# Kernel tuning notes

Hardware: AMD Instinct MI355X
Metric: run time of the kernel (lower is better)

## Reference

```python
import jax, jax.numpy as jnp
import numpy as np

NEG_SLOPE = 0.2

def _smlp(x, w, b):
    # torch nn.Linear convention: y = x @ w.T + b, then leaky_relu(0.2)
    return jax.nn.leaky_relu(x @ w.T + b, NEG_SLOPE)

_gather = jax.vmap(lambda a, i: a[i])  # (N,C),(N,k) -> (N,k,C), vmapped over batch

def _lfa(points, feats, idx, w, b):
    # points: (B,N,3), feats: (B,N,F_D), idx: (B,N,k)
    knn_p = _gather(points, idx)                      # (B,N,k,3)
    rel = points[:, :, None, :] - knn_p               # (B,N,k,3)
    dist = jnp.linalg.norm(rel, axis=-1, keepdims=True)
    geo = jnp.concatenate([rel, dist], axis=-1)       # (B,N,k,4)
    mlp = _smlp(geo, w, b)                            # (B,N,k,d)
    knn_f = _gather(feats, idx)                       # (B,N,k,F_D)
    return jnp.concatenate([mlp, knn_f], axis=-1).mean(axis=2)  # (B,N,d+F_D)

def setup_inputs() -> dict:
    key = jax.random.key(0)
    ks = jax.random.split(key, 12)
    B, N, K, D = 2, 65536, 32, 64
    pts = jax.random.normal(ks[0], (B, N, 3), jnp.float32)
    feats = jax.random.normal(ks[1], (B, N, D), jnp.float32)
    idx = jax.random.randint(ks[2], (B, N, K), 0, N)
    def lin(k, o, i):
        bound = 1.0 / np.sqrt(i)
        kw, kb = jax.random.split(k)
        return (jax.random.uniform(kw, (o, i), jnp.float32, -bound, bound),
                jax.random.uniform(kb, (o,), jnp.float32, -bound, bound))
    w_init, b_init = lin(ks[3], D // 4, D)
    w_lfa1, b_lfa1 = lin(ks[4], D // 4, 4)
    w_lfa2, b_lfa2 = lin(ks[5], D // 2, 4)
    w_final, b_final = lin(ks[6], D, D)
    w_res, b_res = lin(ks[7], D, D)
    return {"points": pts, "features": feats, "knn_indices": idx,
            "w_init": w_init, "b_init": b_init,
            "w_lfa1": w_lfa1, "b_lfa1": b_lfa1,
            "w_lfa2": w_lfa2, "b_lfa2": b_lfa2,
            "w_final": w_final, "b_final": b_final,
            "w_res": w_res, "b_res": b_res}

def reference(points, features, knn_indices, w_init, b_init,
              w_lfa1, b_lfa1, w_lfa2, b_lfa2,
              w_final, b_final, w_res, b_res):
    x = _smlp(features, w_init, b_init)               # (B,N,16)
    x = _lfa(points, x, knn_indices, w_lfa1, b_lfa1)  # (B,N,32)
    x = _lfa(points, x, knn_indices, w_lfa2, b_lfa2)  # (B,N,64)
    x = _smlp(x, w_final, b_final)                    # (B,N,64)
    residual = _smlp(features, w_res, b_res)          # (B,N,64)
    return x + residual
```

## Files before the change

kernel.cpp:

```cpp
#include <hip/hip_runtime.h>
#include <math.h>

#define NPTS 65536

typedef unsigned short ushort_t;
typedef unsigned int uint_t;
typedef __attribute__((ext_vector_type(8))) short bf16x8;
typedef __attribute__((ext_vector_type(4))) float f32x4;
typedef __attribute__((ext_vector_type(2))) float f32x2;

__device__ __forceinline__ float lrelu(float x) {
  return fmaxf(x, 0.2f * x);
}
__device__ __forceinline__ f32x2 lrelu2(f32x2 s) {
  return __builtin_elementwise_max(s, s * 0.2f);
}
__device__ __forceinline__ float fast_sqrtf(float x) {
  return __builtin_amdgcn_sqrtf(x);
}
__device__ __forceinline__ ushort_t f2b(float f) {
  union { float f; uint_t u; } v; v.f = f;
  uint_t u = v.u + (0x7fffu + ((v.u >> 16) & 1u));
  return (ushort_t)(u >> 16);
}
__device__ __forceinline__ float b2f_lo(uint_t u) {
  union { uint_t u; float f; } v; v.u = u << 16; return v.f;
}
__device__ __forceinline__ float b2f_hi(uint_t u) {
  union { uint_t u; float f; } v; v.u = u & 0xffff0000u; return v.f;
}
__device__ __forceinline__ bf16x8 cvt8(const float* p) {
  float4 a = ((const float4*)p)[0];
  float4 b = ((const float4*)p)[1];
  float f[8] = {a.x, a.y, a.z, a.w, b.x, b.y, b.z, b.w};
  bf16x8 r;
#pragma unroll
  for (int j = 0; j < 8; ++j) r[j] = (short)f2b(f[j]);
  return r;
}

__device__ __forceinline__ int swz_pbase(int ppb) {
  int bid = blockIdx.x;
  if ((int)gridDim.x * ppb == 2 * NPTS) {
    int g = bid >> 3, x = bid & 7;
    return (x >> 2) * NPTS + (g * 4 + (x & 3)) * ppb;
  }
  return bid * ppb;
}

__global__ __launch_bounds__(256) void k_init(
    const float* __restrict__ feats, const float* __restrict__ w,
    const float* __restrict__ bia, ushort_t* __restrict__ x1,
    const float* __restrict__ pts, float4* __restrict__ pts4,
    const float* __restrict__ wf, const float* __restrict__ wr,
    ushort_t* __restrict__ wfb, ushort_t* __restrict__ wrb, int BN) {
  __shared__ float wt[64 * 16];
  int t = threadIdx.x;
  if (blockIdx.x < 2) {
    const float* src = blockIdx.x ? wr : wf;
    ushort_t* dst = blockIdx.x ? wrb : wfb;
    for (int e = t; e < 4096; e += 256) dst[e] = f2b(src[e]);
  }
  for (int e = t; e < 1024; e += 256) {
    int o = e >> 6, i = e & 63;
    wt[i * 16 + o] = w[e];
  }
  __syncthreads();
  int p = blockIdx.x * 256 + t;
  if (p >= BN) return;
  const float* pp = pts + (size_t)p * 3;
  pts4[p] = make_float4(pp[0], pp[1], pp[2], 0.0f);
  float acc[16];
#pragma unroll
  for (int o = 0; o < 16; ++o) acc[o] = bia[o];
  const float4* xr4 = (const float4*)(feats + (size_t)p * 64);
#pragma unroll 4
  for (int i4 = 0; i4 < 16; ++i4) {
    float4 xv = xr4[i4];
    float xs[4] = {xv.x, xv.y, xv.z, xv.w};
#pragma unroll
    for (int s = 0; s < 4; ++s) {
      float xi = xs[s];
      const float4* w4 = (const float4*)&wt[(i4 * 4 + s) * 16];
#pragma unroll
      for (int q = 0; q < 4; ++q) {
        float4 wv = w4[q];
        acc[q * 4 + 0] = fmaf(xi, wv.x, acc[q * 4 + 0]);
        acc[q * 4 + 1] = fmaf(xi, wv.y, acc[q * 4 + 1]);
        acc[q * 4 + 2] = fmaf(xi, wv.z, acc[q * 4 + 2]);
        acc[q * 4 + 3] = fmaf(xi, wv.w, acc[q * 4 + 3]);
      }
    }
  }
  union { ushort_t u[16]; uint4 v[2]; } pk;
#pragma unroll
  for (int o = 0; o < 16; ++o) pk.u[o] = f2b(lrelu(acc[o]));
  uint4* op = (uint4*)(x1 + (size_t)p * 16);
  op[0] = pk.v[0];
  op[1] = pk.v[1];
}

__global__ __launch_bounds__(256) void k_lfa1g(
    const float4* __restrict__ pts4, const ushort_t* __restrict__ fin,
    const int* __restrict__ idx, const float* __restrict__ w1,
    const float* __restrict__ b1, const float* __restrict__ w2,
    const float* __restrict__ b2, ushort_t* __restrict__ x2out,
    ushort_t* __restrict__ g2out, int BN) {
  int t = threadIdx.x;
  int p = swz_pbase(32) + (t >> 3);
  int sub = t & 7;
  if (p >= BN) return;
  int base = p & ~(NPTS - 1);
  float4 mp = pts4[p];
  const float* w1b = w1 + sub * 8;
  f32x2 w1p[4], b1p;
#pragma unroll
  for (int k = 0; k < 4; ++k) w1p[k] = f32x2{w1b[k], w1b[4 + k]};
  b1p = f32x2{b1[sub * 2], b1[sub * 2 + 1]};
  const float* w2b = w2 + sub * 16;
  f32x2 w2p[2][4], b2p[2];
#pragma unroll
  for (int pr = 0; pr < 2; ++pr) {
#pragma unroll
    for (int k = 0; k < 4; ++k)
      w2p[pr][k] = f32x2{w2b[pr * 8 + k], w2b[pr * 8 + 4 + k]};
    b2p[pr] = f32x2{b2[sub * 4 + pr * 2], b2[sub * 4 + pr * 2 + 1]};
  }
  f32x2 m1 = {0.f, 0.f}, f1 = {0.f, 0.f};
  f32x2 m2[2] = {{0.f, 0.f}, {0.f, 0.f}};
  const int4* iv4 = (const int4*)(idx + (size_t)p * 32);
#pragma unroll 2
  for (int kk = 0; kk < 8; ++kk) {
    int4 iv = iv4[kk];
    int js[4] = {iv.x, iv.y, iv.z, iv.w};
#pragma unroll
    for (int u = 0; u < 4; ++u) {
      int j = base + js[u];
      float4 pj = pts4[j];
      uint_t fv = *((const uint_t*)(fin + (size_t)j * 16) + sub);
      float rx = mp.x - pj.x, ry = mp.y - pj.y, rz = mp.z - pj.z;
      float d = fast_sqrtf(fmaf(rx, rx, fmaf(ry, ry, rz * rz)));
      f32x2 vx = {rx, rx}, vy = {ry, ry}, vz = {rz, rz}, vd = {d, d};
      f32x2 s = __builtin_elementwise_fma(vd, w1p[3], b1p);
      s = __builtin_elementwise_fma(vz, w1p[2], s);
      s = __builtin_elementwise_fma(vy, w1p[1], s);
      s = __builtin_elementwise_fma(vx, w1p[0], s);
      m1 += lrelu2(s);
#pragma unroll
      for (int pr = 0; pr < 2; ++pr) {
        f32x2 s2 = __builtin_elementwise_fma(vd, w2p[pr][3], b2p[pr]);
        s2 = __builtin_elementwise_fma(vz, w2p[pr][2], s2);
        s2 = __builtin_elementwise_fma(vy, w2p[pr][1], s2);
        s2 = __builtin_elementwise_fma(vx, w2p[pr][0], s2);
        m2[pr] += lrelu2(s2);
      }
      f1 += f32x2{b2f_lo(fv), b2f_hi(fv)};
    }
  }
  const float inv = 1.0f / 32.0f;
  ushort_t* orow = x2out + (size_t)p * 32;
  union { ushort_t u[2]; uint_t v; } pm, pf;
  pm.u[0] = f2b(m1.x * inv); pm.u[1] = f2b(m1.y * inv);
  pf.u[0] = f2b(f1.x * inv); pf.u[1] = f2b(f1.y * inv);
  ((uint_t*)orow)[sub] = pm.v;
  ((uint_t*)orow)[8 + sub] = pf.v;
  union { ushort_t u[4]; uint2 v; } pg;
  pg.u[0] = f2b(m2[0].x * inv); pg.u[1] = f2b(m2[0].y * inv);
  pg.u[2] = f2b(m2[1].x * inv); pg.u[3] = f2b(m2[1].y * inv);
  ((uint2*)(g2out + (size_t)p * 32))[sub] = pg.v;
}

__global__ __launch_bounds__(256) void k_lfa2f(
    const ushort_t* __restrict__ fin, const int* __restrict__ idx,
    const ushort_t* __restrict__ g2, const float* __restrict__ feats,
    const ushort_t* __restrict__ wfb, const float* __restrict__ bfi,
    const ushort_t* __restrict__ wrb, const float* __restrict__ bri,
    float* __restrict__ out, int BN) {
  int t = threadIdx.x;
  int lane = t & 63, wave = t >> 6;
  int n = lane & 15, quad = lane >> 4;
  int wbase = swz_pbase(64) + wave * 16;
  int p0 = wbase + n;
  int p = p0 < BN ? p0 : BN - 1;
  int base = p & ~(NPTS - 1);
  f32x2 fa[4];
#pragma unroll
  for (int o = 0; o < 4; ++o) fa[o] = f32x2{0.f, 0.f};
  const int4* iv4 = (const int4*)(idx + (size_t)p * 32);
#pragma unroll 8
  for (int kk = 0; kk < 8; ++kk) {
    int4 iv = iv4[kk];
    int js[4] = {iv.x, iv.y, iv.z, iv.w};
#pragma unroll
    for (int u = 0; u < 4; ++u) {
      int j = base + js[u];
      uint4 fv = *((const uint4*)(fin + (size_t)j * 32) + quad);
      fa[0] += f32x2{b2f_lo(fv.x), b2f_hi(fv.x)};
      fa[1] += f32x2{b2f_lo(fv.y), b2f_hi(fv.y)};
      fa[2] += f32x2{b2f_lo(fv.z), b2f_hi(fv.z)};
      fa[3] += f32x2{b2f_lo(fv.w), b2f_hi(fv.w)};
    }
  }
  const float inv = 1.0f / 32.0f;
  bf16x8 Ax0 = *((const bf16x8*)(g2 + (size_t)p * 32 + quad * 8));
  bf16x8 Ax1;
#pragma unroll
  for (int o = 0; o < 4; ++o) {
    Ax1[o * 2 + 0] = (short)f2b(fa[o].x * inv);
    Ax1[o * 2 + 1] = (short)f2b(fa[o].y * inv);
  }
  const float* af = feats + (size_t)p * 64 + quad * 8;
  bf16x8 Af0 = cvt8(af), Af1 = cvt8(af + 32);
#pragma unroll
  for (int nt = 0; nt < 4; ++nt) {
    int woff = (nt * 16 + n) * 64 + quad * 8;
    bf16x8 Bf0 = *((const bf16x8*)(wfb + woff));
    bf16x8 Bf1 = *((const bf16x8*)(wfb + woff + 32));
    f32x4 accx = {0.f, 0.f, 0.f, 0.f};
    accx = __builtin_amdgcn_mfma_f32_16x16x32_bf16(Ax0, Bf0, accx, 0, 0, 0);
    accx = __builtin_amdgcn_mfma_f32_16x16x32_bf16(Ax1, Bf1, accx, 0, 0, 0);
    bf16x8 Br0 = *((const bf16x8*)(wrb + woff));
    bf16x8 Br1 = *((const bf16x8*)(wrb + woff + 32));
    f32x4 accr = {0.f, 0.f, 0.f, 0.f};
    accr = __builtin_amdgcn_mfma_f32_16x16x32_bf16(Af0, Br0, accr, 0, 0, 0);
    accr = __builtin_amdgcn_mfma_f32_16x16x32_bf16(Af1, Br1, accr, 0, 0, 0);
    float bvf = bfi[nt * 16 + n];
    float bvr = bri[nt * 16 + n];
#pragma unroll
    for (int r = 0; r < 4; ++r) {
      int row = wbase + quad * 4 + r;
      if (row < BN)
        out[(size_t)row * 64 + nt * 16 + n] =
            lrelu(accx[r] + bvf) + lrelu(accr[r] + bvr);
    }
  }
}

extern "C" void kernel_launch(void* const* d_in, const int* in_sizes, int n_in,
                              void* d_out, int out_size, void* d_ws, size_t ws_size,
                              hipStream_t stream) {
  const float* pts    = (const float*)d_in[0];
  const float* feats  = (const float*)d_in[1];
  const int*   idx    = (const int*)d_in[2];
  const float* w_init = (const float*)d_in[3];
  const float* b_init = (const float*)d_in[4];
  const float* w_l1   = (const float*)d_in[5];
  const float* b_l1   = (const float*)d_in[6];
  const float* w_l2   = (const float*)d_in[7];
  const float* b_l2   = (const float*)d_in[8];
  const float* w_f    = (const float*)d_in[9];
  const float* b_f    = (const float*)d_in[10];
  const float* w_r    = (const float*)d_in[11];
  const float* b_r    = (const float*)d_in[12];
  float* out = (float*)d_out;

  int BN = in_sizes[2] / 32;
  ushort_t* x1 = (ushort_t*)d_ws;
  ushort_t* x2 = x1 + (size_t)BN * 16;
  float4* pts4 = (float4*)(x2 + (size_t)BN * 32);
  ushort_t* wfb = (ushort_t*)(pts4 + BN);
  ushort_t* wrb = wfb + 4096;
  ushort_t* g2 = wrb + 4096;

  int blocks_pt = (BN + 255) / 256;
  int blocks_l1 = (BN + 31) / 32;
  int blocks_l2 = (BN + 63) / 64;

  k_init<<<blocks_pt, 256, 0, stream>>>(feats, w_init, b_init, x1, pts, pts4,
                                        w_f, w_r, wfb, wrb, BN);
  k_lfa1g<<<blocks_l1, 256, 0, stream>>>(pts4, x1, idx, w_l1, b_l1, w_l2, b_l2,
                                         x2, g2, BN);
  k_lfa2f<<<blocks_l2, 256, 0, stream>>>(x2, idx, g2, feats, wfb, b_f, wrb, b_r,
                                         out, BN);
}
```

Measured before the change: 223.2 us.

## Interleave point coords and init features into one 64-byte gather record

Packs each point's xyz (float4) and its 16 bf16 init features into a single 64-byte record, so each neighbor gather in the first LFA kernel touches one cache line instead of two separate arrays. The unroll factor of the neighbor loop in k_lfa1g is also raised from 2 to 4. k_lfa2f is launched with 128-thread blocks covering 32 points each instead of 256 threads covering 64. The padded record wastes 16 bytes per point and increases workspace writes in k_init.

```diff
diff --git a/kernel.cpp b/kernel.cpp
--- a/kernel.cpp
+++ b/kernel.cpp
@@ -50,8 +50,8 @@
 
 __global__ __launch_bounds__(256) void k_init(
     const float* __restrict__ feats, const float* __restrict__ w,
-    const float* __restrict__ bia, ushort_t* __restrict__ x1,
-    const float* __restrict__ pts, float4* __restrict__ pts4,
+    const float* __restrict__ bia, const float* __restrict__ pts,
+    char* __restrict__ tbl,
     const float* __restrict__ wf, const float* __restrict__ wr,
     ushort_t* __restrict__ wfb, ushort_t* __restrict__ wrb, int BN) {
   __shared__ float wt[64 * 16];
@@ -68,8 +68,6 @@
   __syncthreads();
   int p = blockIdx.x * 256 + t;
   if (p >= BN) return;
-  const float* pp = pts + (size_t)p * 3;
-  pts4[p] = make_float4(pp[0], pp[1], pp[2], 0.0f);
   float acc[16];
 #pragma unroll
   for (int o = 0; o < 16; ++o) acc[o] = bia[o];
@@ -95,23 +93,24 @@
   union { ushort_t u[16]; uint4 v[2]; } pk;
 #pragma unroll
   for (int o = 0; o < 16; ++o) pk.u[o] = f2b(lrelu(acc[o]));
-  uint4* op = (uint4*)(x1 + (size_t)p * 16);
-  op[0] = pk.v[0];
-  op[1] = pk.v[1];
+  char* rec = tbl + (size_t)p * 64;
+  const float* pp = pts + (size_t)p * 3;
+  *(float4*)rec = make_float4(pp[0], pp[1], pp[2], 0.0f);
+  *(uint4*)(rec + 16) = pk.v[0];
+  *(uint4*)(rec + 32) = pk.v[1];
 }
 
 __global__ __launch_bounds__(256) void k_lfa1g(
-    const float4* __restrict__ pts4, const ushort_t* __restrict__ fin,
-    const int* __restrict__ idx, const float* __restrict__ w1,
-    const float* __restrict__ b1, const float* __restrict__ w2,
-    const float* __restrict__ b2, ushort_t* __restrict__ x2out,
-    ushort_t* __restrict__ g2out, int BN) {
+    const char* __restrict__ tbl, const int* __restrict__ idx,
+    const float* __restrict__ w1, const float* __restrict__ b1,
+    const float* __restrict__ w2, const float* __restrict__ b2,
+    ushort_t* __restrict__ x2out, ushort_t* __restrict__ g2out, int BN) {
   int t = threadIdx.x;
   int p = swz_pbase(32) + (t >> 3);
   int sub = t & 7;
   if (p >= BN) return;
   int base = p & ~(NPTS - 1);
-  float4 mp = pts4[p];
+  float4 mp = *(const float4*)(tbl + (size_t)p * 64);
   const float* w1b = w1 + sub * 8;
   f32x2 w1p[4], b1p;
 #pragma unroll
@@ -126,18 +125,20 @@
       w2p[pr][k] = f32x2{w2b[pr * 8 + k], w2b[pr * 8 + 4 + k]};
     b2p[pr] = f32x2{b2[sub * 4 + pr * 2], b2[sub * 4 + pr * 2 + 1]};
   }
+  int loff = 16 + sub * 4;
   f32x2 m1 = {0.f, 0.f}, f1 = {0.f, 0.f};
   f32x2 m2[2] = {{0.f, 0.f}, {0.f, 0.f}};
   const int4* iv4 = (const int4*)(idx + (size_t)p * 32);
-#pragma unroll 2
+#pragma unroll 4
   for (int kk = 0; kk < 8; ++kk) {
     int4 iv = iv4[kk];
     int js[4] = {iv.x, iv.y, iv.z, iv.w};
 #pragma unroll
     for (int u = 0; u < 4; ++u) {
       int j = base + js[u];
-      float4 pj = pts4[j];
-      uint_t fv = *((const uint_t*)(fin + (size_t)j * 16) + sub);
+      const char* rj = tbl + (size_t)j * 64;
+      float4 pj = *(const float4*)rj;
+      uint_t fv = *(const uint_t*)(rj + loff);
       float rx = mp.x - pj.x, ry = mp.y - pj.y, rz = mp.z - pj.z;
       float d = fast_sqrtf(fmaf(rx, rx, fmaf(ry, ry, rz * rz)));
       f32x2 vx = {rx, rx}, vy = {ry, ry}, vz = {rz, rz}, vd = {d, d};
@@ -170,7 +171,7 @@
   ((uint2*)(g2out + (size_t)p * 32))[sub] = pg.v;
 }
 
-__global__ __launch_bounds__(256) void k_lfa2f(
+__global__ __launch_bounds__(128) void k_lfa2f(
     const ushort_t* __restrict__ fin, const int* __restrict__ idx,
     const ushort_t* __restrict__ g2, const float* __restrict__ feats,
     const ushort_t* __restrict__ wfb, const float* __restrict__ bfi,
@@ -179,7 +180,7 @@
   int t = threadIdx.x;
   int lane = t & 63, wave = t >> 6;
   int n = lane & 15, quad = lane >> 4;
-  int wbase = swz_pbase(64) + wave * 16;
+  int wbase = swz_pbase(32) + wave * 16;
   int p0 = wbase + n;
   int p = p0 < BN ? p0 : BN - 1;
   int base = p & ~(NPTS - 1);
@@ -255,21 +256,20 @@
   float* out = (float*)d_out;
 
   int BN = in_sizes[2] / 32;
-  ushort_t* x1 = (ushort_t*)d_ws;
-  ushort_t* x2 = x1 + (size_t)BN * 16;
-  float4* pts4 = (float4*)(x2 + (size_t)BN * 32);
-  ushort_t* wfb = (ushort_t*)(pts4 + BN);
+  char* tbl = (char*)d_ws;
+  ushort_t* x2 = (ushort_t*)(tbl + (size_t)BN * 64);
+  ushort_t* g2 = x2 + (size_t)BN * 32;
+  ushort_t* wfb = g2 + (size_t)BN * 32;
   ushort_t* wrb = wfb + 4096;
-  ushort_t* g2 = wrb + 4096;
 
   int blocks_pt = (BN + 255) / 256;
   int blocks_l1 = (BN + 31) / 32;
-  int blocks_l2 = (BN + 63) / 64;
-
-  k_init<<<blocks_pt, 256, 0, stream>>>(feats, w_init, b_init, x1, pts, pts4,
+  int blocks_l2 = (BN + 31) / 32;
+
+  k_init<<<blocks_pt, 256, 0, stream>>>(feats, w_init, b_init, pts, tbl,
                                         w_f, w_r, wfb, wrb, BN);
-  k_lfa1g<<<blocks_l1, 256, 0, stream>>>(pts4, x1, idx, w_l1, b_l1, w_l2, b_l2,
+  k_lfa1g<<<blocks_l1, 256, 0, stream>>>(tbl, idx, w_l1, b_l1, w_l2, b_l2,
                                          x2, g2, BN);
-  k_lfa2f<<<blocks_l2, 256, 0, stream>>>(x2, idx, g2, feats, wfb, b_f, wrb, b_r,
+  k_lfa2f<<<blocks_l2, 128, 0, stream>>>(x2, idx, g2, feats, wfb, b_f, wrb, b_r,
                                          out, BN);
 }
```

Measured after the change: 232.3 us. 1.04x slower.
